# Kernel tuning notes

Hardware: AMD Instinct MI355X
Metric: run time of the kernel (lower is better)

Reference implementation:

```python
import jax, jax.numpy as jnp
import numpy as np

B, N, D_M, H, D_K, R, GRID = 2, 2048, 128, 8, 16, 4, 64


def setup_inputs() -> dict:
    key = jax.random.key(0)
    ks = jax.random.split(key, 12)
    z = jax.random.normal(ks[0], (B, N, D_M), dtype=jnp.float32)
    patch_token = jax.random.normal(ks[1], (B, 1, D_M), dtype=jnp.float32)
    positions = jax.random.randint(ks[2], (B, N, 2), 0, GRID, dtype=jnp.int32)
    alive_mask = (jax.random.uniform(ks[3], (B, N, 1)) > 0.1).astype(jnp.float32)
    s = 0.02
    Wq = jax.random.normal(ks[4], (D_M, H * D_K), dtype=jnp.float32) * s
    Wk = jax.random.normal(ks[5], (D_M, H * D_K), dtype=jnp.float32) * s
    Wv = jax.random.normal(ks[6], (D_M, H * D_K), dtype=jnp.float32) * s
    Wo = jax.random.normal(ks[7], (H * D_K, D_M), dtype=jnp.float32) * s
    bq = jnp.zeros((H * D_K,), jnp.float32)
    bk = jnp.zeros((H * D_K,), jnp.float32)
    bv = jnp.zeros((H * D_K,), jnp.float32)
    bo = jnp.zeros((D_M,), jnp.float32)
    rel_bias = jax.random.normal(ks[8], (H, 2 * R + 1, 2 * R + 1), dtype=jnp.float32) * s
    return {"z": z, "patch_token": patch_token, "positions": positions, "alive_mask": alive_mask,
            "Wq": Wq, "bq": bq, "Wk": Wk, "bk": bk, "Wv": Wv, "bv": bv, "Wo": Wo, "bo": bo,
            "rel_bias": rel_bias}


def reference(z, patch_token, positions, alive_mask, Wq, bq, Wk, bk, Wv, bv, Wo, bo, rel_bias):
    B_, N_, _ = z.shape
    H_ = rel_bias.shape[0]
    R_ = (rel_bias.shape[1] - 1) // 2
    dk = Wq.shape[1] // H_
    alive = alive_mask                                   # [B,N,1] float 0/1
    z_a = z * alive
    tokens = jnp.concatenate([z_a, patch_token], axis=1)  # [B,N+1,d_m]
    q = (z_a @ Wq + bq).reshape(B_, N_, H_, dk).transpose(0, 2, 1, 3)       # [B,H,N,dk]
    k = (tokens @ Wk + bk).reshape(B_, N_ + 1, H_, dk).transpose(0, 2, 1, 3)
    v = (tokens @ Wv + bv).reshape(B_, N_ + 1, H_, dk).transpose(0, 2, 1, 3)
    q = q * alive[:, None]                               # [B,1,N,1] broadcast
    logits = jnp.einsum('bhnd,bhmd->bhnm', q, k) / jnp.sqrt(jnp.float32(dk))  # [B,H,N,N+1]
    # Chebyshev mask (delta = pos_i - pos_j)
    delta = positions[:, :, None, :] - positions[:, None, :, :]               # [B,N,N,2]
    cheb = jnp.maximum(jnp.abs(delta[..., 0]), jnp.abs(delta[..., 1]))
    alive_j = alive[:, :, 0] > 0
    not_self = ~jnp.eye(N_, dtype=bool)
    allowed = (cheb <= R_) & alive_j[:, None, :] & not_self[None]
    mask_agents = jnp.where(allowed, 0.0, -1e9).astype(jnp.float32)           # [B,N,N]
    # Relative-position bias (torch uses delta_rel = pos_j - pos_i = -delta)
    dx = -delta[..., 0] + R_
    dy = -delta[..., 1] + R_
    valid = (dx >= 0) & (dx <= 2 * R_) & (dy >= 0) & (dy <= 2 * R_)
    flat = jnp.clip(dx, 0, 2 * R_) * (2 * R_ + 1) + jnp.clip(dy, 0, 2 * R_)   # [B,N,N] int
    table = rel_bias.reshape(H_, -1)
    rel = jnp.moveaxis(jnp.take(table, flat, axis=1), 0, 1)                   # [B,H,N,N]
    rel = rel * valid[:, None].astype(jnp.float32)
    add = mask_agents[:, None] + rel                                          # [B,H,N,N]
    logits = logits + jnp.pad(add, ((0, 0), (0, 0), (0, 0), (0, 1)))          # patch col: mask 0, no bias
    logits = jnp.where(alive[:, None] > 0, logits, -1e9)                      # dead queries
    attn = jax.nn.softmax(logits, axis=-1)
    out = jnp.einsum('bhnm,bhmd->bhnd', attn, v)
    out = out.transpose(0, 2, 1, 3).reshape(B_, N_, H_ * dk)
    out = (out @ Wo + bo) * alive
    return out
```

## Files before the change

kernel.cpp:

```cpp
#include <hip/hip_runtime.h>
#include <hip/hip_fp16.h>
#include <math.h>

#define BB 2
#define NN 2048
#define NP1 2049
#define DM 128
#define NH 8
#define DK 16
#define RWIN 4
#define GRID_W 64
#define QPB 4
#define CAND_PQ 160

__device__ __forceinline__ void unpack8(uint4 r, float* f) {
    float2 t;
    t = __half22float2(*(const __half2*)&r.x); f[0] = t.x; f[1] = t.y;
    t = __half22float2(*(const __half2*)&r.y); f[2] = t.x; f[3] = t.y;
    t = __half22float2(*(const __half2*)&r.z); f[4] = t.x; f[5] = t.y;
    t = __half22float2(*(const __half2*)&r.w); f[6] = t.x; f[7] = t.y;
}


#define QKV_ROWS 16

__global__ __launch_bounds__(384) void qkv_kernel(
    const float* __restrict__ z, const float* __restrict__ patch,
    const float* __restrict__ Wq, const float* __restrict__ bq,
    const float* __restrict__ Wk, const float* __restrict__ bk,
    const float* __restrict__ Wv, const float* __restrict__ bv,
    float* __restrict__ q, __half* __restrict__ k, __half* __restrict__ v) {
    __shared__ float zrow[QKV_ROWS][DM];
    const int tid = threadIdx.x;
    const int mat = tid >> 7;
    const int rem = tid & 127;
    const int cg = rem & 31;
    const int rs = rem >> 5;
    const int r0 = blockIdx.x * QKV_ROWS;
    const int NROWS = BB * NP1;

    for (int t = tid; t < QKV_ROWS * DM / 4; t += 384) {
        int r = t >> 5, q4 = t & 31;
        int row = r0 + r;
        float4 val = make_float4(0.f, 0.f, 0.f, 0.f);
        if (row < NROWS) {
            int b = row / NP1, ti = row % NP1;
            const float* src = (ti < NN) ? (z + ((size_t)b * NN + ti) * DM)
                                         : (patch + (size_t)b * DM);
            val = ((const float4*)src)[q4];
        }
        *((float4*)&zrow[r][q4 * 4]) = val;
    }
    __syncthreads();

    const float* W    = (mat == 0) ? Wq : (mat == 1) ? Wk : Wv;
    const float* bias = (mat == 0) ? bq : (mat == 1) ? bk : bv;

    float4 acc[4];
#pragma unroll
    for (int rr = 0; rr < 4; ++rr) acc[rr] = make_float4(0.f, 0.f, 0.f, 0.f);

#pragma unroll 2
    for (int kk4 = 0; kk4 < DM; kk4 += 4) {
        float4 zv0 = *((const float4*)&zrow[rs][kk4]);
        float4 zv1 = *((const float4*)&zrow[rs + 4][kk4]);
        float4 zv2 = *((const float4*)&zrow[rs + 8][kk4]);
        float4 zv3 = *((const float4*)&zrow[rs + 12][kk4]);
        const float* zp0 = (const float*)&zv0;
        const float* zp1 = (const float*)&zv1;
        const float* zp2 = (const float*)&zv2;
        const float* zp3 = (const float*)&zv3;
#pragma unroll
        for (int t = 0; t < 4; ++t) {
            float4 w4 = *((const float4*)(W + (size_t)(kk4 + t) * DM + cg * 4));
            float z0 = zp0[t], z1 = zp1[t], z2 = zp2[t], z3 = zp3[t];
            acc[0].x = fmaf(z0, w4.x, acc[0].x); acc[0].y = fmaf(z0, w4.y, acc[0].y);
            acc[0].z = fmaf(z0, w4.z, acc[0].z); acc[0].w = fmaf(z0, w4.w, acc[0].w);
            acc[1].x = fmaf(z1, w4.x, acc[1].x); acc[1].y = fmaf(z1, w4.y, acc[1].y);
            acc[1].z = fmaf(z1, w4.z, acc[1].z); acc[1].w = fmaf(z1, w4.w, acc[1].w);
            acc[2].x = fmaf(z2, w4.x, acc[2].x); acc[2].y = fmaf(z2, w4.y, acc[2].y);
            acc[2].z = fmaf(z2, w4.z, acc[2].z); acc[2].w = fmaf(z2, w4.w, acc[2].w);
            acc[3].x = fmaf(z3, w4.x, acc[3].x); acc[3].y = fmaf(z3, w4.y, acc[3].y);
            acc[3].z = fmaf(z3, w4.z, acc[3].z); acc[3].w = fmaf(z3, w4.w, acc[3].w);
        }
    }
    float4 b4 = *((const float4*)(bias + cg * 4));

#pragma unroll
    for (int rr = 0; rr < 4; ++rr) {
        int row = r0 + rs + rr * 4;
        if (row >= NROWS) break;
        float4 val;
        val.x = acc[rr].x + b4.x; val.y = acc[rr].y + b4.y;
        val.z = acc[rr].z + b4.z; val.w = acc[rr].w + b4.w;
        int b = row / NP1, ti = row % NP1;
        if (mat == 0) {
            if (ti < NN) ((float4*)(q + ((size_t)b * NN + ti) * DM))[cg] = val;
        } else {
            __half2 p0 = __floats2half2_rn(val.x, val.y);
            __half2 p1 = __floats2half2_rn(val.z, val.w);
            uint2 st;
            st.x = *(unsigned int*)&p0;
            st.y = *(unsigned int*)&p1;
            __half* dst = ((mat == 1) ? k : v) + ((size_t)b * NP1 + ti) * DM;
            ((uint2*)dst)[cg] = st;
        }
    }
}


__global__ __launch_bounds__(256) void attn_out_kernel(
    const float* __restrict__ q, const __half* __restrict__ k, const __half* __restrict__ v,
    const int* __restrict__ positions, const float* __restrict__ alive,
    const float* __restrict__ rel_bias, const float* __restrict__ Wo,
    const float* __restrict__ bo, float* __restrict__ out) {
    const int tid = threadIdx.x;
    const int qq = tid >> 6;
    const int l6 = tid & 63;
    const int h = l6 >> 3;
    const int s = l6 & 7;
    const int r0 = blockIdx.x * QPB;
    const int b = r0 >> 11;
    const int bi = r0 + qq;

    __shared__ float sbias[NH * 81];
    __shared__ int   spx[QPB], spy[QPB];
    __shared__ float sal[QPB];
    __shared__ int   mcount[QPB];
    __shared__ int   cand[QPB][CAND_PQ];
    __shared__ float srow[QPB][DM];
    __shared__ float4 pw[QPB][QPB][32];

    if (tid < QPB) {
        mcount[tid] = 0;
        int gbi = r0 + tid;
        spx[tid] = positions[gbi * 2 + 0];
        spy[tid] = positions[gbi * 2 + 1];
        sal[tid] = alive[gbi];
    }
    if (tid < NH * 81 / 4) ((float4*)sbias)[tid] = ((const float4*)rel_bias)[tid];

    const __half* kb = k + (size_t)b * NP1 * DM;
    const __half* vb = v + (size_t)b * NP1 * DM;

    float qf[16];
    {
        const float4* qr = (const float4*)(q + (size_t)bi * DM + h * DK);
#pragma unroll
        for (int e = 0; e < 4; ++e) {
            float4 t4 = qr[e];
            qf[e * 4 + 0] = t4.x * 0.25f; qf[e * 4 + 1] = t4.y * 0.25f;
            qf[e * 4 + 2] = t4.z * 0.25f; qf[e * 4 + 3] = t4.w * 0.25f;
        }
    }

    __syncthreads();

    int qx[QPB], qy[QPB], qi[QPB];
    float qa[QPB];
#pragma unroll
    for (int u = 0; u < QPB; ++u) {
        qx[u] = spx[u]; qy[u] = spy[u]; qa[u] = sal[u];
        qi[u] = (r0 + u) & (NN - 1);
    }

    {
        const int2* pb = (const int2*)(positions + (size_t)b * NN * 2);
        const float* ab = alive + (size_t)b * NN;
#pragma unroll
        for (int u = 0; u < NN / 256; ++u) {
            int j = u * 256 + tid;
            int2 pj = pb[j];
            float aj = ab[j];
            if (aj > 0.5f) {
                int packed = j | (pj.x << 16) | (pj.y << 24);
#pragma unroll
                for (int qn = 0; qn < QPB; ++qn) {
                    int dx = pj.x - qx[qn]; dx = dx < 0 ? -dx : dx;
                    int dy = pj.y - qy[qn]; dy = dy < 0 ? -dy : dy;
                    int ch = dx > dy ? dx : dy;
                    if (ch <= RWIN && j != qi[qn] && qa[qn] > 0.5f) {
                        int slot = atomicAdd(&mcount[qn], 1);
                        if (slot < CAND_PQ) cand[qn][slot] = packed;
                    }
                }
            }
        }
    }
    __syncthreads();
    int M = mcount[qq]; if (M > CAND_PQ) M = CAND_PQ;
    const int pix = qx[qq], piy = qy[qq];

    float l = 0.f;
    float o[16];
#pragma unroll
    for (int e = 0; e < 16; ++e) o[e] = 0.f;

    if (s == 0) {
        const uint4* kr = (const uint4*)(kb + (size_t)NN * DM + h * DK);
        uint4 ka = kr[0], kb4 = kr[1];
        const uint4* vr = (const uint4*)(vb + (size_t)NN * DM + h * DK);
        uint4 va = vr[0], vb4 = vr[1];
        float kf[16], vf[16];
        unpack8(ka, kf); unpack8(kb4, kf + 8);
        unpack8(va, vf); unpack8(vb4, vf + 8);
        float d = 0.f;
#pragma unroll
        for (int e = 0; e < 16; ++e) d = fmaf(qf[e], kf[e], d);
        float p = __expf(d);
        l += p;
#pragma unroll
        for (int e = 0; e < 16; ++e) o[e] = fmaf(p, vf[e], o[e]);
    }

    for (int t = s; t < M; t += 16) {
        const int t1 = t + 8;
        const bool has1 = t1 < M;
        int packed0 = cand[qq][t];
        int packed1 = has1 ? cand[qq][t1] : packed0;
        int j0 = packed0 & 0xFFFF;
        int j1 = packed1 & 0xFFFF;

        const uint4* kr0 = (const uint4*)(kb + (size_t)j0 * DM + h * DK);
        const uint4* vr0 = (const uint4*)(vb + (size_t)j0 * DM + h * DK);
        const uint4* kr1 = (const uint4*)(kb + (size_t)j1 * DM + h * DK);
        const uint4* vr1 = (const uint4*)(vb + (size_t)j1 * DM + h * DK);
        uint4 k0a = kr0[0], k0b = kr0[1];
        uint4 v0a = vr0[0], v0b = vr0[1];
        uint4 k1a = kr1[0], k1b = kr1[1];
        uint4 v1a = vr1[0], v1b = vr1[1];

        {
            float kf[16], vf[16];
            unpack8(k0a, kf); unpack8(k0b, kf + 8);
            unpack8(v0a, vf); unpack8(v0b, vf + 8);
            float d = 0.f;
#pragma unroll
            for (int e = 0; e < 16; ++e) d = fmaf(qf[e], kf[e], d);
            int pjx = (packed0 >> 16) & 0xFF;
            int pjy = (packed0 >> 24) & 0xFF;
            float bias = sbias[h * 81 + (pjx - pix + RWIN) * 9 + (pjy - piy + RWIN)];
            float p = __expf(d + bias);
            l += p;
#pragma unroll
            for (int e = 0; e < 16; ++e) o[e] = fmaf(p, vf[e], o[e]);
        }
        if (has1) {
            float kf[16], vf[16];
            unpack8(k1a, kf); unpack8(k1b, kf + 8);
            unpack8(v1a, vf); unpack8(v1b, vf + 8);
            float d = 0.f;
#pragma unroll
            for (int e = 0; e < 16; ++e) d = fmaf(qf[e], kf[e], d);
            int pjx = (packed1 >> 16) & 0xFF;
            int pjy = (packed1 >> 24) & 0xFF;
            float bias = sbias[h * 81 + (pjx - pix + RWIN) * 9 + (pjy - piy + RWIN)];
            float p = __expf(d + bias);
            l += p;
#pragma unroll
            for (int e = 0; e < 16; ++e) o[e] = fmaf(p, vf[e], o[e]);
        }
    }

    float r2_0, r2_1;
    {
        float r8[8];
        const bool hi4 = (s & 4) != 0;
#pragma unroll
        for (int e = 0; e < 8; ++e) {
            float a = o[e]     + __shfl_xor(o[e],     4, 64);
            float bq_ = o[e + 8] + __shfl_xor(o[e + 8], 4, 64);
            r8[e] = hi4 ? bq_ : a;
        }
        float r4[4];
        const bool hi2 = (s & 2) != 0;
#pragma unroll
        for (int e = 0; e < 4; ++e) {
            float a = r8[e]     + __shfl_xor(r8[e],     2, 64);
            float bq_ = r8[e + 4] + __shfl_xor(r8[e + 4], 2, 64);
            r4[e] = hi2 ? bq_ : a;
        }
        const bool hi1 = (s & 1) != 0;
#pragma unroll
        for (int e = 0; e < 2; ++e) {
            float a = r4[e]     + __shfl_xor(r4[e],     1, 64);
            float bq_ = r4[e + 2] + __shfl_xor(r4[e + 2], 1, 64);
            float r = hi1 ? bq_ : a;
            if (e == 0) r2_0 = r; else r2_1 = r;
        }
        l += __shfl_xor(l, 1, 64);
        l += __shfl_xor(l, 2, 64);
        l += __shfl_xor(l, 4, 64);
    }
    {
        float linv = 1.f / l;
        float2 st;
        st.x = r2_0 * linv;
        st.y = r2_1 * linv;
        *((float2*)&srow[qq][h * DK + s * 2]) = st;
    }
    __syncthreads();

    {
        const int wv = qq;
        const int ks = l6 >> 5;
        const int m  = l6 & 31;
        const int kbase = wv * 32 + ks * 16;
        float4 acc[QPB];
#pragma unroll
        for (int oq = 0; oq < QPB; ++oq) acc[oq] = make_float4(0.f, 0.f, 0.f, 0.f);
#pragma unroll
        for (int r = 0; r < 16; ++r) {
            const int kk = kbase + r;
            float4 w4 = *((const float4*)(Wo + (size_t)kk * DM + m * 4));
#pragma unroll
            for (int oq = 0; oq < QPB; ++oq) {
                float sv = srow[oq][kk];
                acc[oq].x = fmaf(sv, w4.x, acc[oq].x);
                acc[oq].y = fmaf(sv, w4.y, acc[oq].y);
                acc[oq].z = fmaf(sv, w4.z, acc[oq].z);
                acc[oq].w = fmaf(sv, w4.w, acc[oq].w);
            }
        }
#pragma unroll
        for (int oq = 0; oq < QPB; ++oq) {
            acc[oq].x += __shfl_xor(acc[oq].x, 32, 64);
            acc[oq].y += __shfl_xor(acc[oq].y, 32, 64);
            acc[oq].z += __shfl_xor(acc[oq].z, 32, 64);
            acc[oq].w += __shfl_xor(acc[oq].w, 32, 64);
        }
        if (ks == 0) {
#pragma unroll
            for (int oq = 0; oq < QPB; ++oq) pw[wv][oq][m] = acc[oq];
        }
    }
    __syncthreads();

    if (tid < QPB * 32) {
        const int oq = tid >> 5;
        const int m  = tid & 31;
        float4 s0 = pw[0][oq][m], s1 = pw[1][oq][m];
        float4 s2 = pw[2][oq][m], s3 = pw[3][oq][m];
        float ga = sal[oq] > 0.5f ? 1.f : 0.f;
        float4 b4 = *((const float4*)(bo + m * 4));
        float4 r;
        r.x = (s0.x + s1.x + s2.x + s3.x + b4.x) * ga;
        r.y = (s0.y + s1.y + s2.y + s3.y + b4.y) * ga;
        r.z = (s0.z + s1.z + s2.z + s3.z + b4.z) * ga;
        r.w = (s0.w + s1.w + s2.w + s3.w + b4.w) * ga;
        ((float4*)(out + (size_t)(r0 + oq) * DM))[m] = r;
    }
}

extern "C" void kernel_launch(void* const* d_in, const int* in_sizes, int n_in,
                              void* d_out, int out_size, void* d_ws, size_t ws_size,
                              hipStream_t stream) {
    const float* z         = (const float*)d_in[0];
    const float* patch     = (const float*)d_in[1];
    const int*   positions = (const int*)d_in[2];
    const float* alive     = (const float*)d_in[3];
    const float* Wq        = (const float*)d_in[4];
    const float* bq        = (const float*)d_in[5];
    const float* Wk        = (const float*)d_in[6];
    const float* bk        = (const float*)d_in[7];
    const float* Wv        = (const float*)d_in[8];
    const float* bv        = (const float*)d_in[9];
    const float* Wo        = (const float*)d_in[10];
    const float* bo        = (const float*)d_in[11];
    const float* rel_bias  = (const float*)d_in[12];
    float* out = (float*)d_out;

    char* ws = (char*)d_ws;
    size_t off = 0;
    auto alloc = [&](size_t bytes) -> void* {
        void* p = ws + off;
        off += (bytes + 255) & ~(size_t)255;
        return p;
    };
    float*  q = (float*)alloc((size_t)BB * NN * DM * 4);
    __half* k = (__half*)alloc((size_t)BB * NP1 * DM * 2);
    __half* v = (__half*)alloc((size_t)BB * NP1 * DM * 2);

    qkv_kernel<<<(BB * NP1 + QKV_ROWS - 1) / QKV_ROWS, 384, 0, stream>>>(z, patch, Wq, bq, Wk, bk, Wv, bv, q, k, v);
    attn_out_kernel<<<(BB * NN) / QPB, 256, 0, stream>>>(q, k, v, positions, alive, rel_bias, Wo, bo, out);
}
```

Measured before the change: 115.1 us.

## Split QKV projection reduction across two thread halves with shared-memory combine

The QKV projection kernel now processes 8 rows per block with 768 threads. Each matrix's work is split into two halves over the K dimension, and the partial sums are combined through shared memory before bias and store. This doubles the number of blocks and threads to raise parallelism and latency hiding in the projection stage. The cost is an extra barrier, extra shared memory, and more total weight loads per output row.

```diff
diff --git a/kernel.cpp b/kernel.cpp
--- a/kernel.cpp
+++ b/kernel.cpp
@@ -22,25 +22,27 @@
 }
 
 
-#define QKV_ROWS 16
-
-__global__ __launch_bounds__(384) void qkv_kernel(
+#define QKV_ROWS 8
+
+__global__ __launch_bounds__(768) void qkv_kernel(
     const float* __restrict__ z, const float* __restrict__ patch,
     const float* __restrict__ Wq, const float* __restrict__ bq,
     const float* __restrict__ Wk, const float* __restrict__ bk,
     const float* __restrict__ Wv, const float* __restrict__ bv,
     float* __restrict__ q, __half* __restrict__ k, __half* __restrict__ v) {
     __shared__ float zrow[QKV_ROWS][DM];
+    __shared__ float pacc[3][QKV_ROWS][DM];
     const int tid = threadIdx.x;
-    const int mat = tid >> 7;
-    const int rem = tid & 127;
+    const int mat  = tid >> 8;
+    const int half = (tid >> 7) & 1;
+    const int rem  = tid & 127;
     const int cg = rem & 31;
     const int rs = rem >> 5;
     const int r0 = blockIdx.x * QKV_ROWS;
     const int NROWS = BB * NP1;
 
-    for (int t = tid; t < QKV_ROWS * DM / 4; t += 384) {
-        int r = t >> 5, q4 = t & 31;
+    if (tid < QKV_ROWS * DM / 4) {
+        int r = tid >> 5, q4 = tid & 31;
         int row = r0 + r;
         float4 val = make_float4(0.f, 0.f, 0.f, 0.f);
         if (row < NROWS) {
@@ -55,55 +57,58 @@
 
     const float* W    = (mat == 0) ? Wq : (mat == 1) ? Wk : Wv;
     const float* bias = (mat == 0) ? bq : (mat == 1) ? bk : bv;
-
-    float4 acc[4];
-#pragma unroll
-    for (int rr = 0; rr < 4; ++rr) acc[rr] = make_float4(0.f, 0.f, 0.f, 0.f);
-
-#pragma unroll 2
-    for (int kk4 = 0; kk4 < DM; kk4 += 4) {
+    const int k0 = half * 64;
+
+    float4 a0 = make_float4(0.f, 0.f, 0.f, 0.f);
+    float4 a1 = make_float4(0.f, 0.f, 0.f, 0.f);
+#pragma unroll 4
+    for (int kk4 = k0; kk4 < k0 + 64; kk4 += 4) {
         float4 zv0 = *((const float4*)&zrow[rs][kk4]);
         float4 zv1 = *((const float4*)&zrow[rs + 4][kk4]);
-        float4 zv2 = *((const float4*)&zrow[rs + 8][kk4]);
-        float4 zv3 = *((const float4*)&zrow[rs + 12][kk4]);
         const float* zp0 = (const float*)&zv0;
         const float* zp1 = (const float*)&zv1;
-        const float* zp2 = (const float*)&zv2;
-        const float* zp3 = (const float*)&zv3;
 #pragma unroll
         for (int t = 0; t < 4; ++t) {
             float4 w4 = *((const float4*)(W + (size_t)(kk4 + t) * DM + cg * 4));
-            float z0 = zp0[t], z1 = zp1[t], z2 = zp2[t], z3 = zp3[t];
-            acc[0].x = fmaf(z0, w4.x, acc[0].x); acc[0].y = fmaf(z0, w4.y, acc[0].y);
-            acc[0].z = fmaf(z0, w4.z, acc[0].z); acc[0].w = fmaf(z0, w4.w, acc[0].w);
-            acc[1].x = fmaf(z1, w4.x, acc[1].x); acc[1].y = fmaf(z1, w4.y, acc[1].y);
-            acc[1].z = fmaf(z1, w4.z, acc[1].z); acc[1].w = fmaf(z1, w4.w, acc[1].w);
-            acc[2].x = fmaf(z2, w4.x, acc[2].x); acc[2].y = fmaf(z2, w4.y, acc[2].y);
-            acc[2].z = fmaf(z2, w4.z, acc[2].z); acc[2].w = fmaf(z2, w4.w, acc[2].w);
-            acc[3].x = fmaf(z3, w4.x, acc[3].x); acc[3].y = fmaf(z3, w4.y, acc[3].y);
-            acc[3].z = fmaf(z3, w4.z, acc[3].z); acc[3].w = fmaf(z3, w4.w, acc[3].w);
-        }
-    }
-    float4 b4 = *((const float4*)(bias + cg * 4));
-
-#pragma unroll
-    for (int rr = 0; rr < 4; ++rr) {
-        int row = r0 + rs + rr * 4;
-        if (row >= NROWS) break;
-        float4 val;
-        val.x = acc[rr].x + b4.x; val.y = acc[rr].y + b4.y;
-        val.z = acc[rr].z + b4.z; val.w = acc[rr].w + b4.w;
-        int b = row / NP1, ti = row % NP1;
-        if (mat == 0) {
-            if (ti < NN) ((float4*)(q + ((size_t)b * NN + ti) * DM))[cg] = val;
-        } else {
-            __half2 p0 = __floats2half2_rn(val.x, val.y);
-            __half2 p1 = __floats2half2_rn(val.z, val.w);
-            uint2 st;
-            st.x = *(unsigned int*)&p0;
-            st.y = *(unsigned int*)&p1;
-            __half* dst = ((mat == 1) ? k : v) + ((size_t)b * NP1 + ti) * DM;
-            ((uint2*)dst)[cg] = st;
+            float z0 = zp0[t], z1 = zp1[t];
+            a0.x = fmaf(z0, w4.x, a0.x); a0.y = fmaf(z0, w4.y, a0.y);
+            a0.z = fmaf(z0, w4.z, a0.z); a0.w = fmaf(z0, w4.w, a0.w);
+            a1.x = fmaf(z1, w4.x, a1.x); a1.y = fmaf(z1, w4.y, a1.y);
+            a1.z = fmaf(z1, w4.z, a1.z); a1.w = fmaf(z1, w4.w, a1.w);
+        }
+    }
+
+    if (half == 1) {
+        *((float4*)&pacc[mat][rs][cg * 4])     = a0;
+        *((float4*)&pacc[mat][rs + 4][cg * 4]) = a1;
+    }
+    __syncthreads();
+
+    if (half == 0) {
+        float4 p0 = *((const float4*)&pacc[mat][rs][cg * 4]);
+        float4 p1 = *((const float4*)&pacc[mat][rs + 4][cg * 4]);
+        float4 b4 = *((const float4*)(bias + cg * 4));
+        float4 o0 = make_float4(a0.x + p0.x + b4.x, a0.y + p0.y + b4.y,
+                                a0.z + p0.z + b4.z, a0.w + p0.w + b4.w);
+        float4 o1 = make_float4(a1.x + p1.x + b4.x, a1.y + p1.y + b4.y,
+                                a1.z + p1.z + b4.z, a1.w + p1.w + b4.w);
+#pragma unroll
+        for (int rr = 0; rr < 2; ++rr) {
+            int row = r0 + rs + rr * 4;
+            if (row >= NROWS) break;
+            float4 val = rr ? o1 : o0;
+            int b = row / NP1, ti = row % NP1;
+            if (mat == 0) {
+                if (ti < NN) ((float4*)(q + ((size_t)b * NN + ti) * DM))[cg] = val;
+            } else {
+                __half2 p0h = __floats2half2_rn(val.x, val.y);
+                __half2 p1h = __floats2half2_rn(val.z, val.w);
+                uint2 st;
+                st.x = *(unsigned int*)&p0h;
+                st.y = *(unsigned int*)&p1h;
+                __half* dst = ((mat == 1) ? k : v) + ((size_t)b * NP1 + ti) * DM;
+                ((uint2*)dst)[cg] = st;
+            }
         }
     }
 }
@@ -381,6 +386,6 @@
     __half* k = (__half*)alloc((size_t)BB * NP1 * DM * 2);
     __half* v = (__half*)alloc((size_t)BB * NP1 * DM * 2);
 
-    qkv_kernel<<<(BB * NP1 + QKV_ROWS - 1) / QKV_ROWS, 384, 0, stream>>>(z, patch, Wq, bq, Wk, bk, Wv, bv, q, k, v);
+    qkv_kernel<<<(BB * NP1 + QKV_ROWS - 1) / QKV_ROWS, 768, 0, stream>>>(z, patch, Wq, bq, Wk, bk, Wv, bv, q, k, v);
     attn_out_kernel<<<(BB * NN) / QPB, 256, 0, stream>>>(q, k, v, positions, alive, rel_bias, Wo, bo, out);
 }
```

After: 118.0 us. 2.6% more time.
